# Kernel tuning notes

Measured on AMD Instinct MI355X. Metric: run time of the kernel, lower is better.

## Reference

```python
import jax, jax.numpy as jnp
import numpy as np

H = 512          # HIDDEN_DIM
W = 480          # WINDOWWIDTH
NL = 8           # NUMLABELS (output_dim)
STEPS = W // 15  # 32 decoder steps
ATT = W // 16    # 30 attention positions
B = 4            # window batch
L = 12           # per-frame sequence length
D_IN = 32        # input_dim
N = B * W        # 1920 frame sequences


def _lstm(x, Wih, Whh, bih, bhh):
    # x: [T, Bn, Din] -> per-step hidden/cell states [T, Bn, Hd] (torch LSTM gate order i,f,g,o)
    xp = x @ Wih.T + (bih + bhh)
    h0 = jnp.zeros((x.shape[1], Whh.shape[1]), x.dtype)
    def step(carry, xt):
        h, c = carry
        g = xt + h @ Whh.T
        i, f, gg, o = jnp.split(g, 4, axis=-1)
        c = jax.nn.sigmoid(f) * c + jax.nn.sigmoid(i) * jnp.tanh(gg)
        h = jax.nn.sigmoid(o) * jnp.tanh(c)
        return (h, c), (h, c)
    _, (hs, cs) = jax.lax.scan(step, (h0, h0), xp)
    return hs, cs


def _bilstm(x, Wf, Uf, bf, cf, Wb, Ub, bb, cb):
    # x: [Bt, T, D] batch_first; returns ([Bt, T, 2H], h_fwd_final, h_bwd_final)
    xt = jnp.swapaxes(x, 0, 1)
    hf, _ = _lstm(xt, Wf, Uf, bf, cf)
    hb, _ = _lstm(xt[::-1], Wb, Ub, bb, cb)
    out = jnp.concatenate([hf, hb[::-1]], axis=-1)
    return jnp.swapaxes(out, 0, 1), hf[-1], hb[-1]


def _forward(xs, xlengths, enc_Wih, enc_Whh, enc_bih, enc_bhh,
             penc_Wih_f, penc_Whh_f, penc_bih_f, penc_bhh_f,
             penc_Wih_b, penc_Whh_b, penc_bih_b, penc_bhh_b,
             attn_W, attn_b, comb_W, comb_b,
             gru_Wih, gru_Whh, gru_bih, gru_bhh, out_W, out_b):
    # frame-level encoder: packed sequences -> (h, c) at each sequence's true length
    hs, cs = _lstm(xs, enc_Wih, enc_Whh, enc_bih, enc_bhh)   # [L, N, H] each
    idx = xlengths - 1
    ar = jnp.arange(N)
    ctx = jnp.concatenate([hs[idx, ar], cs[idx, ar]], axis=-1)  # [N, 2H]
    ctx = ctx.reshape(B, W // 2, 4 * H)
    # pyramidal BiLSTM stack (dropout is identity at eval)
    out = ctx
    hf = hb = None
    for i in range(4):
        out, hf, hb = _bilstm(ctx, penc_Wih_f[i], penc_Whh_f[i], penc_bih_f[i], penc_bhh_f[i],
                              penc_Wih_b[i], penc_Whh_b[i], penc_bih_b[i], penc_bhh_b[i])
        if i < 3:
            ctx = out.reshape(B, W // (2 ** (i + 2)), 4 * H)
    enc_out = out                                   # [B, ATT, 2H]
    hidden0 = jnp.concatenate([hf, hb], axis=-1)    # [B, 2H]

    def dstep(carry, _):
        inp, h = carry                              # [B, NL], [B, 2H]
        aw = jax.nn.softmax(jnp.concatenate([inp, h], axis=-1) @ attn_W.T + attn_b, axis=-1)
        ctxv = jnp.einsum('bt,btd->bd', aw, enc_out)
        x = jax.nn.relu(jnp.concatenate([inp, ctxv], axis=-1) @ comb_W.T + comb_b)
        # torch GRU cell (gate order r, z, n)
        gi = x @ gru_Wih.T + gru_bih
        gh = h @ gru_Whh.T + gru_bhh
        ir, iz, inn = jnp.split(gi, 3, axis=-1)
        hr, hz, hn = jnp.split(gh, 3, axis=-1)
        r = jax.nn.sigmoid(ir + hr)
        z = jax.nn.sigmoid(iz + hz)
        n = jnp.tanh(inn + r * hn)
        hnew = (1.0 - z) * n + z * h
        logp = jax.nn.log_softmax(hnew @ out_W.T + out_b, axis=-1)
        return (logp, hnew), logp                   # free-running: next input = log-probs

    inp0 = jnp.zeros((B, NL), xs.dtype)
    _, outs = jax.lax.scan(dstep, (inp0, hidden0), None, length=STEPS)  # [STEPS, B, NL]
    return jnp.swapaxes(outs, 0, 1).reshape(B * STEPS, NL)


def setup_inputs() -> dict:
    key = jax.random.key(0)
    ks = jax.random.split(key, 24)
    s = 0.03
    def nrm(k, shape):
        return jax.random.normal(k, shape, dtype=jnp.float32) * s
    return {
        'xs': jax.random.normal(ks[0], (L, N, D_IN), dtype=jnp.float32),
        'xlengths': jax.random.randint(ks[1], (N,), 1, L + 1, dtype=jnp.int32),
        'enc_Wih': nrm(ks[2], (4 * H, D_IN)),
        'enc_Whh': nrm(ks[3], (4 * H, H)),
        'enc_bih': nrm(ks[4], (4 * H,)),
        'enc_bhh': nrm(ks[5], (4 * H,)),
        'penc_Wih_f': nrm(ks[6], (4, 4 * H, 4 * H)),
        'penc_Whh_f': nrm(ks[7], (4, 4 * H, H)),
        'penc_bih_f': nrm(ks[8], (4, 4 * H)),
        'penc_bhh_f': nrm(ks[9], (4, 4 * H)),
        'penc_Wih_b': nrm(ks[10], (4, 4 * H, 4 * H)),
        'penc_Whh_b': nrm(ks[11], (4, 4 * H, H)),
        'penc_bih_b': nrm(ks[12], (4, 4 * H)),
        'penc_bhh_b': nrm(ks[13], (4, 4 * H)),
        'attn_W': nrm(ks[14], (ATT, 2 * H + NL)),
        'attn_b': nrm(ks[15], (ATT,)),
        'comb_W': nrm(ks[16], (H, 2 * H + NL)),
        'comb_b': nrm(ks[17], (H,)),
        'gru_Wih': nrm(ks[18], (3 * 2 * H, H)),
        'gru_Whh': nrm(ks[19], (3 * 2 * H, 2 * H)),
        'gru_bih': nrm(ks[20], (3 * 2 * H,)),
        'gru_bhh': nrm(ks[21], (3 * 2 * H,)),
        'out_W': nrm(ks[22], (NL, 2 * H)),
        'out_b': nrm(ks[23], (NL,)),
    }


def reference(xs, xlengths, enc_Wih, enc_Whh, enc_bih, enc_bhh,
              penc_Wih_f, penc_Whh_f, penc_bih_f, penc_bhh_f,
              penc_Wih_b, penc_Whh_b, penc_bih_b, penc_bhh_b,
              attn_W, attn_b, comb_W, comb_b,
              gru_Wih, gru_Whh, gru_bih, gru_bhh, out_W, out_b):
    return _forward(xs, xlengths, enc_Wih, enc_Whh, enc_bih, enc_bhh,
                    penc_Wih_f, penc_Whh_f, penc_bih_f, penc_bhh_f,
                    penc_Wih_b, penc_Whh_b, penc_bih_b, penc_bhh_b,
                    attn_W, attn_b, comb_W, comb_b,
                    gru_Wih, gru_Whh, gru_bih, gru_bhh, out_W, out_b)
```

## Files before the change

kernel.cpp:

```cpp
#include <hip/hip_runtime.h>
#include <stdint.h>

typedef __attribute__((ext_vector_type(8))) __bf16 bf16x8;
typedef __attribute__((ext_vector_type(4))) float f32x4;
typedef __attribute__((ext_vector_type(4))) unsigned u32x4;

#define DEVI static __device__ __forceinline__
#define SENT 0xFFFFFFFFu

DEVI bf16x8 bzero8(){ bf16x8 r;
#pragma unroll
  for (int i=0;i<8;++i) r[i]=(__bf16)0.0f; return r; }

DEVI bf16x8 ld8(const __bf16* p){ return *(const bf16x8*)p; }
DEVI void st8(__bf16* p, bf16x8 v){ *(bf16x8*)p = v; }

DEVI f32x4 MFMA(bf16x8 a, bf16x8 b, f32x4 c){
  return __builtin_amdgcn_mfma_f32_16x16x32_bf16(a, b, c, 0, 0, 0);
}

DEVI float sigf(float x){ return 1.0f/(1.0f+__expf(-x)); }

DEVI void ast(unsigned* p, unsigned v){ __hip_atomic_store(p, v, __ATOMIC_RELAXED, __HIP_MEMORY_SCOPE_AGENT); }

DEVI unsigned packbf(float a, float b){
  union { __bf16 h[2]; unsigned u; } x; x.h[0]=(__bf16)a; x.h[1]=(__bf16)b; return x.u;
}
DEVI float bflo(unsigned u){ return __builtin_bit_cast(float, u<<16); }
DEVI float bfhi(unsigned u){ return __builtin_bit_cast(float, u & 0xffff0000u); }

DEVI unsigned bad4(u32x4 v){ return (v[0]==SENT)|(v[1]==SENT)|(v[2]==SENT)|(v[3]==SENT); }

DEVI u32x4 ald4(const void* p){
  u32x4 v;
  asm volatile("global_load_dwordx4 %0, %1, off sc0 sc1\n\ts_waitcnt vmcnt(0)"
               : "=&v"(v) : "v"(p) : "memory");
  return v;
}
DEVI u32x4 poll4(const void* p){
  u32x4 v = ald4(p);
  while (bad4(v)){ __builtin_amdgcn_s_sleep(1); v = ald4(p); }
  return v;
}
DEVI void ald4x2(const void* p, u32x4& a, u32x4& b){
  asm volatile("global_load_dwordx4 %0, %2, off sc0 sc1\n\t"
               "global_load_dwordx4 %1, %2, off offset:16 sc0 sc1\n\t"
               "s_waitcnt vmcnt(0)"
               : "=&v"(a), "=&v"(b) : "v"(p) : "memory");
}
DEVI void poll4x2(const void* p, u32x4& a, u32x4& b){
  ald4x2(p, a, b);
  while (bad4(a) | bad4(b)){ __builtin_amdgcn_s_sleep(1); ald4x2(p, a, b); }
}

DEVI void packGroup(const float* W, int Nsrc, int Kreal, int NT, __bf16* dst, long g){
  int kt = (int)(g / (NT*64));
  int rem = (int)(g % (NT*64));
  int nt = rem >> 6, ln = rem & 63;
  int row = nt*16 + (ln & 15);
  int col = kt*32 + ((ln >> 4) << 3);
  bf16x8 v = bzero8();
  if (row < Nsrc){
#pragma unroll
    for (int j=0;j<8;++j){ int c = col + j; if (c < Kreal) v[j] = (__bf16)W[(long)row*Kreal + c]; }
  }
  st8(dst + g*8, v);
}

DEVI void packGroupCat(const float* Wih, const float* Whh, __bf16* dst, long g){
  int kt = (int)(g / (128*64));
  int rem = (int)(g % (128*64));
  int nt = rem >> 6, ln = rem & 63;
  int prow = nt*16 + (ln & 15);
  int src = (prow & 3)*512 + (prow >> 2);
  int col = kt*32 + ((ln >> 4) << 3);
  bf16x8 v;
  if (col < 32){
#pragma unroll
    for (int j=0;j<8;++j) v[j] = (__bf16)Wih[(long)src*32 + col + j];
  } else {
#pragma unroll
    for (int j=0;j<8;++j) v[j] = (__bf16)Whh[(long)src*512 + (col-32) + j];
  }
  st8(dst + g*8, v);
}

__global__ void initK(unsigned* bar, unsigned* hb, unsigned* ctx, unsigned* xb){
  int g = blockIdx.x*256 + threadIdx.x;
  if (g < 3072){ bar[g] = 0u; return; }
  g -= 3072;
  if (g < 6144){ hb[2048 + g] = SENT; return; }
  g -= 6144;
  if (g < 8192){ ctx[g] = SENT; return; }
  g -= 8192;
  if (g < 4096){ xb[g] = SENT; return; }
}

__global__ void packSmallK(const float* __restrict__ xs, const float* __restrict__ eWih,
    const float* __restrict__ eWhh, const float* __restrict__ ebih, const float* __restrict__ ebhh,
    const float* __restrict__ attnW, const float* __restrict__ combW,
    __bf16* __restrict__ xsb, __bf16* __restrict__ wcatp, float* __restrict__ biasc,
    __bf16* __restrict__ attnp, __bf16* __restrict__ combp)
{
  long g = (long)blockIdx.x*blockDim.x + threadIdx.x;
  const long nWcat = 17L*128*64;
  const long nXs   = 92160;
  const long nBias = 2048;
  const long nAttn = 33L*2*64;
  const long nComb = 33L*32*64;
  if (g < nWcat){ packGroupCat(eWih, eWhh, wcatp, g); return; }
  g -= nWcat;
  if (g < nXs){
    const float* s = xs + g*8; bf16x8 v;
#pragma unroll
    for (int j=0;j<8;++j) v[j] = (__bf16)s[j];
    st8(xsb + g*8, v); return;
  }
  g -= nXs;
  if (g < nBias){ int src = ((int)g & 3)*512 + ((int)g >> 2); biasc[g] = ebih[src] + ebhh[src]; return; }
  g -= nBias;
  if (g < nAttn){ packGroup(attnW, 30, 1032, 2, attnp, g); return; }
  g -= nAttn;
  if (g < nComb){ packGroup(combW, 512, 1032, 32, combp, g); return; }
}

__global__ void packPencK(const float* __restrict__ Wf, const float* __restrict__ Wb,
    const float* __restrict__ bihf, const float* __restrict__ bhhf,
    const float* __restrict__ bihb, const float* __restrict__ bhhb,
    __bf16* __restrict__ pf, __bf16* __restrict__ pb, float* __restrict__ bsum,
    unsigned* __restrict__ hpy)
{
  long g = (long)blockIdx.x*blockDim.x + threadIdx.x;
  const long nW = 64L*128*64;
  if (g < nW){ packGroup(Wf, 2048, 2048, 128, pf, g); return; }
  g -= nW;
  if (g < nW){ packGroup(Wb, 2048, 2048, 128, pb, g); return; }
  g -= nW;
  if (g < 2048){ bsum[g] = bihf[g] + bhhf[g]; return; }
  g -= 2048;
  if (g < 2048){ bsum[2048+g] = bihb[g] + bhhb[g]; return; }
  g -= 2048;
  if (g < 8192){
    hpy[g] = ((g >> 10) & 3) ? SENT : 0u;
  }
}

__global__ __launch_bounds__(256, 1) void encStepK(
    const __bf16* __restrict__ xsb,
    __bf16* __restrict__ henc,
    float* __restrict__ cenc,
    const __bf16* __restrict__ wcatp,
    const float* __restrict__ biasc,
    const int* __restrict__ xlen,
    __bf16* __restrict__ ctx,
    int t)
{
  __shared__ float glds[64][260];
  const int tid = threadIdx.x;
  const int w = tid >> 6, ln = tid & 63;
  const int m0 = blockIdx.x * 64;
  const int nb = blockIdx.y;
  f32x4 acc[16];
#pragma unroll
  for (int i=0;i<16;++i) acc[i] = (f32x4){0.f,0.f,0.f,0.f};

  const int arow = m0 + w*16 + (ln & 15);
  const int kc = (ln >> 4) << 3;
  const int ktEnd = (t == 0) ? 1 : 17;
  for (int kt = 0; kt < ktEnd; ++kt){
    bf16x8 a;
    if (kt == 0) a = ld8(xsb + ((long)t*1920 + arow)*32 + kc);
    else         a = ld8(henc + (long)arow*512 + (kt-1)*32 + kc);
    const __bf16* bp = wcatp + (((long)kt*128 + nb*16)*64 + ln)*8;
#pragma unroll
    for (int n2 = 0; n2 < 16; ++n2){
      bf16x8 b = ld8(bp + (long)n2*512);
      acc[n2] = MFMA(a, b, acc[n2]);
    }
  }
  const int r4 = (ln >> 4) << 2;
#pragma unroll
  for (int n2 = 0; n2 < 16; ++n2){
#pragma unroll
    for (int r = 0; r < 4; ++r)
      glds[w*16 + r4 + r][n2*16 + (ln & 15)] = acc[n2][r];
  }
  __syncthreads();
  for (int it = 0; it < 16; ++it){
    int idx = tid + it*256;
    int mrow = idx >> 6, hcl = idx & 63;
    int n = m0 + mrow;
    int hcg = nb*64 + hcl;
    float ig = glds[mrow][hcl*4+0] + biasc[nb*256 + hcl*4+0];
    float fg = glds[mrow][hcl*4+1] + biasc[nb*256 + hcl*4+1];
    float gg = glds[mrow][hcl*4+2] + biasc[nb*256 + hcl*4+2];
    float og = glds[mrow][hcl*4+3] + biasc[nb*256 + hcl*4+3];
    float c_old = (t == 0) ? 0.0f : cenc[(long)n*512 + hcg];
    float cn = sigf(fg)*c_old + sigf(ig)*tanhf(gg);
    float h  = sigf(og)*tanhf(cn);
    cenc[(long)n*512 + hcg] = cn;
    henc[(long)n*512 + hcg] = (__bf16)h;
    if (xlen[n] - 1 == t){
      ctx[(long)n*1024 + hcg]       = (__bf16)h;
      ctx[(long)n*1024 + 512 + hcg] = (__bf16)cn;
    }
  }
}

__global__ __launch_bounds__(1024) void pencInK(
   const __bf16* __restrict__ inb,
   const __bf16* __restrict__ wpf, const __bf16* __restrict__ wpb,
   const float* __restrict__ bsum,
   float* __restrict__ xpf, float* __restrict__ xpb,
   int M)
{
  const int tid = threadIdx.x, ln = tid & 63, wv = tid >> 6;
  const int rg = wv >> 2, cg = wv & 3;
  const int dir = blockIdx.z;
  const int m0 = blockIdx.x*64 + rg*16;
  const int nb = blockIdx.y;
  const __bf16* wp = dir ? wpb : wpf;
  float* xp = dir ? xpb : xpf;
  const float* bs = bsum + dir*2048;
  f32x4 acc[4];
#pragma unroll
  for (int i=0;i<4;++i) acc[i] = (f32x4){0.f,0.f,0.f,0.f};
  const int arow = m0 + (ln & 15);
  const int kc = (ln >> 4) << 3;
  const bool aok = arow < M;
  for (int kt = 0; kt < 64; ++kt){
    bf16x8 a = aok ? ld8(inb + (long)arow*2048 + kt*32 + kc) : bzero8();
    const __bf16* bp = wp + (((long)kt*128 + nb*16 + cg*4)*64 + ln)*8;
#pragma unroll
    for (int q = 0; q < 4; ++q){
      bf16x8 b = ld8(bp + (long)q*512);
      acc[q] = MFMA(a, b, acc[q]);
    }
  }
  const int r4 = (ln >> 4) << 2;
#pragma unroll
  for (int q = 0; q < 4; ++q){
    int col = (nb*16 + cg*4 + q)*16 + (ln & 15);
#pragma unroll
    for (int r = 0; r < 4; ++r){
      int rowo = m0 + r4 + r;
      if (rowo < M) xp[(long)rowo*2048 + col] = acc[q][r] + bs[col];
    }
  }
}

__global__ __launch_bounds__(256, 1) void pyrRecK(
  const float* __restrict__ WhhF, const float* __restrict__ WhhB,
  const float* __restrict__ xpf, const float* __restrict__ xpb,
  __bf16* __restrict__ hbuf,
  __bf16* __restrict__ outb,
  float* __restrict__ outf,
  float* __restrict__ h0f, __bf16* __restrict__ h0b,
  int T, int isLast)
{
  __shared__ __align__(16) __bf16 WL[128*512];
  __shared__ __align__(16) __bf16 hsL[4*512];
  __shared__ float glds[4][4][32];
  const int tid = threadIdx.x, ln = tid & 63, w = tid >> 6;
  const int bk = blockIdx.x;
  const int dir = bk >> 4, slot = bk & 15;
  const int hc0 = slot * 32;
  const float* Whh = dir ? WhhB : WhhF;
  const float* xp  = dir ? xpb : xpf;
  unsigned* hbu = (unsigned*)hbuf;

  for (int it = 0; it < 32; ++it){
    int g = it*256 + tid;
    int rho = g >> 6, c8 = g & 63;
    int gate = rho >> 5, hcl = rho & 31;
    const float* src = Whh + ((long)(gate*512 + hc0 + hcl))*512 + c8*8;
    bf16x8 v;
#pragma unroll
    for (int j=0;j<8;++j) v[j] = (__bf16)src[j];
    int off = (rho*1024 + c8*16) ^ ((rho & 7) << 4);
    st8((__bf16*)((char*)WL + off), v);
  }

  float cv = 0.0f;
  const int arow = ln & 15;
  const int kc = (ln >> 4) << 3;
  const int rho0 = w*32 + (ln & 15);
  const int rho1 = rho0 + 16;
  for (int t = 0; t < T; ++t){
    int cur = t & 3, nxt = (t+1) & 3, clr = (t+2) & 3;
    int pos = dir ? (T-1-t) : t;
    float x0=0.f, x1=0.f, x2=0.f, x3=0.f;
    if (tid < 128){
      const float* xr = xp + ((long)((tid>>5)*T + pos))*2048 + hc0 + (tid & 31);
      x0 = xr[0]; x1 = xr[512]; x2 = xr[1024]; x3 = xr[1536];
    }
    if (tid < 128 && !(tid & 1)){
      int b = tid >> 5, hcl = tid & 31;
      ast(hbu + ((size_t)(dir*4 + clr)*4 + b)*256 + ((hc0 + hcl) >> 1), SENT);
    }
    {
      u32x4 v = poll4((const char*)hbuf + (size_t)(dir*4 + cur)*4096 + tid*16);
      ((u32x4*)hsL)[tid] = v;
    }
    __syncthreads();
    f32x4 a0 = {0.f,0.f,0.f,0.f}, a1 = {0.f,0.f,0.f,0.f};
#pragma unroll
    for (int kt = 0; kt < 16; ++kt){
      bf16x8 a = (arow < 4) ? ld8(hsL + arow*512 + kt*32 + kc) : bzero8();
      int k2 = (kt*32 + kc)*2;
      bf16x8 b0 = ld8((__bf16*)((char*)WL + ((rho0*1024 + k2) ^ ((rho0 & 7) << 4))));
      bf16x8 b1 = ld8((__bf16*)((char*)WL + ((rho1*1024 + k2) ^ ((rho1 & 7) << 4))));
      a0 = MFMA(a, b0, a0);
      a1 = MFMA(a, b1, a1);
    }
    __syncthreads();
    if (ln < 16){
#pragma unroll
      for (int r=0;r<4;++r){ glds[w][r][ln] = a0[r]; glds[w][r][16+ln] = a1[r]; }
    }
    __syncthreads();
    if (tid < 128){
      int b = tid >> 5, hcl = tid & 31, hcg = hc0 + hcl;
      float ig = glds[0][b][hcl] + x0;
      float fg = glds[1][b][hcl] + x1;
      float gg = glds[2][b][hcl] + x2;
      float og = glds[3][b][hcl] + x3;
      cv = sigf(fg)*cv + sigf(ig)*tanhf(gg);
      float h = sigf(og)*tanhf(cv);
      float hn = __shfl_down(h, 1);
      if (!(hcl & 1))
        ast(hbu + ((size_t)(dir*4 + nxt)*4 + b)*256 + (hcg >> 1), packbf(h, hn));
      if (!isLast){
        outb[((long)(b*T + pos))*1024 + dir*512 + hcg] = (__bf16)h;
      } else {
        outf[((long)(b*T + pos))*1024 + dir*512 + hcg] = h;
        if (t == T-1){
          h0f[b*1024 + dir*512 + hcg] = h;
          h0b[b*1024 + dir*512 + hcg] = (__bf16)h;
        }
      }
    }
  }
}

DEVI bf16x8 dfrag(const __bf16* base, const __bf16* inp, int row, int kt, int kc, int stride){
  if (row >= 4) return bzero8();
  int k = kt*32 + kc;
  if (k == 0) return ld8(inp + row*8);
  int off = k - 8;
  return (off < 1024) ? ld8(base + row*stride + off) : bzero8();
}

__global__ __launch_bounds__(256, 1) void decoderK(
  const float* __restrict__ gWih,
  const float* __restrict__ gWhh,
  const float* __restrict__ gbih, const float* __restrict__ gbhh,
  const float* __restrict__ combBias, const float* __restrict__ attnBias,
  const float* __restrict__ outW, const float* __restrict__ outBias,
  const __bf16* __restrict__ attnP, const __bf16* __restrict__ combP,
  const float* __restrict__ encOut,
  const float* __restrict__ h0f,
  __bf16* __restrict__ HB,
  __bf16* __restrict__ CTXB,
  __bf16* __restrict__ XB,
  float* __restrict__ dout)
{
  __shared__ __align__(16) __bf16 giL[96*512];
  __shared__ __align__(16) __bf16 outWL[8*1024];
  __shared__ __align__(16) __bf16 hL[4*1024];
  __shared__ __align__(16) __bf16 ctxvL[4][1056];
  __shared__ __align__(16) __bf16 xL[4][528];
  __shared__ __bf16 encOutL[4][30][32];
  __shared__ __align__(16) __bf16 inpL[32];
  __shared__ float awL[4][30];
  __shared__ float redL[4][8];
  __shared__ float ghL[3][4][32];
  __shared__ float giO[3][4][32];
  __shared__ float combL[4][4][16];
  __shared__ float biL[3][32], bhL[3][32];
  __shared__ float abL[30], cbL[16];

  const int tid = threadIdx.x, ln = tid & 63, w = tid >> 6;
  const int slot = blockIdx.x;
  const int hc0 = slot * 32;
  unsigned* HBu = (unsigned*)HB;
  unsigned* CTXu = (unsigned*)CTXB;
  unsigned* XBu = (unsigned*)XB;

  for (int it = 0; it < 24; ++it){
    int g = it*256 + tid;
    int rho = g >> 6, c8 = g & 63;
    int gate = rho >> 5, r = rho & 31;
    const float* s = gWih + ((long)(gate*1024 + hc0 + r))*512 + c8*8;
    bf16x8 v;
#pragma unroll
    for (int j=0;j<8;++j) v[j] = (__bf16)s[j];
    st8((__bf16*)((char*)giL + ((rho*1024 + c8*16) ^ ((rho & 7) << 4))), v);
  }
  for (int it = 0; it < 32; ++it){
    int g = it*256 + tid;
    outWL[g] = (__bf16)outW[g];
  }
  for (int idx = tid; idx < 3840; idx += 256){
    int b = idx/960, rem = idx%960;
    int t2 = rem >> 5, dl = rem & 31;
    encOutL[b][t2][dl] = (__bf16)encOut[((long)b*30 + t2)*1024 + hc0 + dl];
  }
  if (tid < 96){
    int g2 = tid >> 5, l = tid & 31;
    biL[g2][l] = gbih[g2*1024 + hc0 + l];
    bhL[g2][l] = gbhh[g2*1024 + hc0 + l];
  }
  if (tid < 30) abL[tid] = attnBias[tid];
  if (tid < 16) cbL[tid] = combBias[slot*16 + tid];

  const int row = ln & 15, kc = (ln >> 4) << 3;
  bf16x8 bigF[66];
  if (w == 0){
#pragma unroll
    for (int nt = 0; nt < 2; ++nt)
#pragma unroll
      for (int kt = 0; kt < 33; ++kt)
        bigF[nt*33 + kt] = ld8(attnP + (((size_t)kt*2 + nt)*64 + ln)*8);
  } else {
    int gate = w - 1;
#pragma unroll
    for (int nt = 0; nt < 2; ++nt)
#pragma unroll
      for (int kt = 0; kt < 32; ++kt){
        const float* s = gWhh + ((long)(gate*1024 + hc0 + nt*16 + row))*1024 + kt*32 + kc;
        bf16x8 v;
#pragma unroll
        for (int j=0;j<8;++j) v[j] = (__bf16)s[j];
        bigF[nt*33 + kt] = v;
      }
  }
  const int kt0c = (w == 0) ? 0 : (w*8 + 1);
  const int nkt = (w == 0) ? 9 : 8;
  bf16x8 combF[9];
#pragma unroll
  for (int i = 0; i < 9; ++i)
    combF[i] = (i < nkt) ? ld8(combP + (((size_t)(kt0c+i)*32 + slot)*64 + ln)*8) : bzero8();

  float hold = 0.f;
  if (tid < 128) hold = h0f[(tid>>5)*1024 + hc0 + (tid & 31)];
  __syncthreads();

  for (int s = 0; s <= 32; ++s){
    int cur = s & 3, nxt = (s+1) & 3, clr = (s+2) & 3;
    if (tid < 64){
      int b = tid >> 4, i = tid & 15;
      ast(HBu  + ((size_t)clr*4 + b)*512 + (hc0 >> 1) + i, SENT);
      ast(CTXu + ((size_t)clr*4 + b)*512 + (hc0 >> 1) + i, SENT);
    }
    if (tid < 32){
      int b = tid >> 3, i = tid & 7;
      ast(XBu + ((size_t)clr*4 + b)*256 + ((slot*16) >> 1) + i, SENT);
    }
    {
      u32x4 q0, q1;
      poll4x2((const char*)HB + (size_t)cur*8192 + tid*32, q0, q1);
      ((u32x4*)hL)[tid*2]   = q0;
      ((u32x4*)hL)[tid*2+1] = q1;
    }
    __syncthreads();
    if (s == 0){
      if (tid < 32) inpL[tid] = (__bf16)0.0f;
      __syncthreads();
    } else {
      int o = tid >> 3, sl = tid & 7;
      int b = o >> 3, l = o & 7;
      const unsigned* hlp = (const unsigned*)hL + b*512 + sl*64;
      const unsigned* wlp = (const unsigned*)outWL + l*512 + sl*64;
      float p = 0.f;
      for (int kk = 0; kk < 64; ++kk){
        unsigned u = hlp[kk], t2 = wlp[kk];
        p += bflo(u)*bflo(t2) + bfhi(u)*bfhi(t2);
      }
      p += __shfl_down(p, 4);
      p += __shfl_down(p, 2);
      p += __shfl_down(p, 1);
      if (sl == 0) redL[b][l] = p + outBias[l];
      __syncthreads();
      if (tid < 4){
        float m = redL[tid][0];
        for (int l2=1;l2<8;++l2) m = fmaxf(m, redL[tid][l2]);
        float sum = 0.f;
        for (int l2=0;l2<8;++l2) sum += __expf(redL[tid][l2]-m);
        float lse = m + __logf(sum);
        for (int l2=0;l2<8;++l2){
          float lp = redL[tid][l2] - lse;
          inpL[tid*8 + l2] = (__bf16)lp;
          if (slot == 0) dout[((long)tid*32 + (s-1))*8 + l2] = lp;
        }
      }
      __syncthreads();
    }
    if (s == 32) break;

    if (w == 0){
      f32x4 a0 = {0.f,0.f,0.f,0.f}, a1 = {0.f,0.f,0.f,0.f};
#pragma unroll
      for (int kt = 0; kt < 33; ++kt){
        bf16x8 a = dfrag(hL, inpL, row, kt, kc, 1024);
        a0 = MFMA(a, bigF[kt], a0);
        a1 = MFMA(a, bigF[33+kt], a1);
      }
      if (ln < 16){
#pragma unroll
        for (int r=0;r<4;++r) awL[r][ln] = a0[r] + abL[ln];
        if (16 + ln < 30){
#pragma unroll
          for (int r=0;r<4;++r) awL[r][16+ln] = a1[r] + abL[16+ln];
        }
      }
    } else {
      f32x4 a0 = {0.f,0.f,0.f,0.f}, a1 = {0.f,0.f,0.f,0.f};
#pragma unroll
      for (int kt = 0; kt < 32; ++kt){
        int k = kt*32 + kc;
        bf16x8 a = (row < 4) ? ld8(hL + row*1024 + k) : bzero8();
        a0 = MFMA(a, bigF[kt], a0);
        a1 = MFMA(a, bigF[33+kt], a1);
      }
      if (ln < 16){
        int gate = w - 1;
#pragma unroll
        for (int r=0;r<4;++r){
          ghL[gate][r][ln] = a0[r];
          ghL[gate][r][16+ln] = a1[r];
        }
      }
    }
    __syncthreads();
    if (tid < 4){
      float m = awL[tid][0];
      for (int t2=1;t2<30;++t2) m = fmaxf(m, awL[tid][t2]);
      float sum = 0.f;
      for (int t2=0;t2<30;++t2){ float e = __expf(awL[tid][t2]-m); awL[tid][t2] = e; sum += e; }
      float inv = 1.0f/sum;
      for (int t2=0;t2<30;++t2) awL[tid][t2] *= inv;
    }
    __syncthreads();
    if (tid < 128){
      int b = tid >> 5, dl = tid & 31;
      float sum = 0.f;
      for (int t2=0;t2<30;++t2) sum += awL[b][t2]*(float)encOutL[b][t2][dl];
      float sn = __shfl_down(sum, 1);
      if (!(dl & 1))
        ast(CTXu + ((size_t)cur*4 + b)*512 + ((hc0 + dl) >> 1), packbf(sum, sn));
    }
    {
      u32x4 q0, q1;
      poll4x2((const char*)CTXB + (size_t)cur*8192 + tid*32, q0, q1);
      u32x4* dst = (u32x4*)((char*)&ctxvL[0][0] + (tid>>6)*2112 + (tid&63)*32);
      dst[0] = q0; dst[1] = q1;
    }
    __syncthreads();
    {
      f32x4 acc = {0.f,0.f,0.f,0.f};
#pragma unroll
      for (int i = 0; i < 9; ++i){
        if (i < nkt){
          bf16x8 a = dfrag(&ctxvL[0][0], inpL, row, kt0c+i, kc, 1056);
          acc = MFMA(a, combF[i], acc);
        }
      }
      if (ln < 16){
#pragma unroll
        for (int r=0;r<4;++r) combL[w][r][ln] = acc[r];
      }
    }
    __syncthreads();
    if (tid < 64){
      int r = tid >> 4, l = tid & 15, col = slot*16 + l;
      float x = combL[0][r][l] + combL[1][r][l] + combL[2][r][l] + combL[3][r][l] + cbL[l];
      x = fmaxf(x, 0.0f);
      float xn = __shfl_down(x, 1);
      if (!(l & 1))
        ast(XBu + ((size_t)cur*4 + r)*256 + (col >> 1), packbf(x, xn));
    }
    {
      u32x4 v = poll4((const char*)XB + (size_t)cur*4096 + tid*16);
      u32x4* dst = (u32x4*)((char*)&xL[0][0] + (tid>>6)*1056 + (tid&63)*16);
      dst[0] = v;
    }
    __syncthreads();
    if (w >= 1){
      int gate = w - 1;
      f32x4 a0 = {0.f,0.f,0.f,0.f}, a1 = {0.f,0.f,0.f,0.f};
#pragma unroll
      for (int kt = 0; kt < 16; ++kt){
        int k = kt*32 + kc;
        bf16x8 a = (row < 4) ? ld8(&xL[row][k]) : bzero8();
        int r0 = gate*32 + row, r1 = r0 + 16;
        bf16x8 b0 = ld8((__bf16*)((char*)giL + ((r0*1024 + k*2) ^ ((r0 & 7) << 4))));
        bf16x8 b1 = ld8((__bf16*)((char*)giL + ((r1*1024 + k*2) ^ ((r1 & 7) << 4))));
        a0 = MFMA(a, b0, a0);
        a1 = MFMA(a, b1, a1);
      }
      if (ln < 16){
#pragma unroll
        for (int r=0;r<4;++r){
          giO[gate][r][ln] = a0[r] + biL[gate][ln];
          giO[gate][r][16+ln] = a1[r] + biL[gate][16+ln];
        }
      }
    }
    __syncthreads();
    if (tid < 128){
      int b = tid >> 5, l = tid & 31, hcg = hc0 + l;
      float rr = sigf(giO[0][b][l] + ghL[0][b][l] + bhL[0][l]);
      float zz = sigf(giO[1][b][l] + ghL[1][b][l] + bhL[1][l]);
      float nn = tanhf(giO[2][b][l] + rr*(ghL[2][b][l] + bhL[2][l]));
      float hnew = (1.0f - zz)*nn + zz*hold;
      hold = hnew;
      float h2 = __shfl_down(hnew, 1);
      if (!(l & 1))
        ast(HBu + ((size_t)nxt*4 + b)*512 + (hcg >> 1), packbf(hnew, h2));
    }
  }
}

static const size_t O_BAR   = 0;
static const size_t O_XSB   = 12288;
static const size_t O_WCATP = 1486848;
static const size_t O_BIASC = 3715072;
static const size_t O_HENC  = 3723264;
static const size_t O_CENC  = 5689344;
static const size_t O_CTX   = 9621504;
static const size_t O_WIHPF = 13553664;
static const size_t O_WIHPB = 21942272;
static const size_t O_BSUM  = 30330880;
static const size_t O_XPF   = 30347264;
static const size_t O_XPB   = 38211584;
static const size_t O_HPYR  = 46075904;
static const size_t O_OUTA  = 46108672;
static const size_t O_OUTB  = 48074752;
static const size_t O_ENCO  = 49057792;
static const size_t O_H0F   = 49549312;
static const size_t O_HB    = 49565696;
static const size_t O_CTXB  = 49598464;
static const size_t O_XB    = 49631232;
static const size_t O_ATTNP = 49647616;
static const size_t O_COMBP = 49715200;

extern "C" void kernel_launch(void* const* d_in, const int* in_sizes, int n_in,
                              void* d_out, int out_size, void* d_ws, size_t ws_size,
                              hipStream_t stream)
{
  const float* xs    = (const float*)d_in[0];
  const int*   xlen  = (const int*)d_in[1];
  const float* eWih  = (const float*)d_in[2];
  const float* eWhh  = (const float*)d_in[3];
  const float* ebih  = (const float*)d_in[4];
  const float* ebhh  = (const float*)d_in[5];
  const float* pWihF = (const float*)d_in[6];
  const float* pWhhF = (const float*)d_in[7];
  const float* pbihF = (const float*)d_in[8];
  const float* pbhhF = (const float*)d_in[9];
  const float* pWihB = (const float*)d_in[10];
  const float* pWhhB = (const float*)d_in[11];
  const float* pbihB = (const float*)d_in[12];
  const float* pbhhB = (const float*)d_in[13];
  const float* attnW = (const float*)d_in[14];
  const float* attnb = (const float*)d_in[15];
  const float* combW = (const float*)d_in[16];
  const float* combb = (const float*)d_in[17];
  const float* gWih  = (const float*)d_in[18];
  const float* gWhh  = (const float*)d_in[19];
  const float* gbih  = (const float*)d_in[20];
  const float* gbhh  = (const float*)d_in[21];
  const float* outW  = (const float*)d_in[22];
  const float* outb  = (const float*)d_in[23];

  char* ws = (char*)d_ws;
  unsigned* BARU  = (unsigned*)(ws + O_BAR);
  __bf16* XSB     = (__bf16*)(ws + O_XSB);
  __bf16* WCATP   = (__bf16*)(ws + O_WCATP);
  float*  BIASC   = (float*)(ws + O_BIASC);
  __bf16* HENC    = (__bf16*)(ws + O_HENC);
  float*  CENC    = (float*)(ws + O_CENC);
  __bf16* CTX     = (__bf16*)(ws + O_CTX);
  __bf16* WIHPF   = (__bf16*)(ws + O_WIHPF);
  __bf16* WIHPB   = (__bf16*)(ws + O_WIHPB);
  float*  BSUM    = (float*)(ws + O_BSUM);
  float*  XPF     = (float*)(ws + O_XPF);
  float*  XPB     = (float*)(ws + O_XPB);
  __bf16* HPYR    = (__bf16*)(ws + O_HPYR);
  __bf16* OUTA    = (__bf16*)(ws + O_OUTA);
  __bf16* OUTB    = (__bf16*)(ws + O_OUTB);
  float*  ENCO    = (float*)(ws + O_ENCO);
  float*  H0F     = (float*)(ws + O_H0F);
  __bf16* HB      = (__bf16*)(ws + O_HB);
  __bf16* CTXB    = (__bf16*)(ws + O_CTXB);
  __bf16* XB      = (__bf16*)(ws + O_XB);
  __bf16* ATTNP   = (__bf16*)(ws + O_ATTNP);
  __bf16* COMBP   = (__bf16*)(ws + O_COMBP);

  initK<<<84, 256, 0, stream>>>(BARU, (unsigned*)HB, (unsigned*)CTXB, (unsigned*)XB);
  packSmallK<<<1193, 256, 0, stream>>>(xs, eWih, eWhh, ebih, ebhh, attnW, combW,
      XSB, WCATP, BIASC, ATTNP, COMBP);

  for (int t = 0; t < 12; ++t)
    encStepK<<<dim3(30, 8), 256, 0, stream>>>(XSB, HENC, CENC, WCATP, BIASC, xlen, CTX, t);

  const int Ts[4] = {240, 120, 60, 30};
  const __bf16* ins[4] = {CTX, OUTA, OUTB, OUTA};
  __bf16* outs[4] = {OUTA, OUTB, OUTA, OUTB};
  for (int L = 0; L < 4; ++L){
    int T = Ts[L];
    packPencK<<<4145, 256, 0, stream>>>(pWihF + (long)L*2048*2048, pWihB + (long)L*2048*2048,
        pbihF + L*2048, pbhhF + L*2048, pbihB + L*2048, pbhhB + L*2048,
        WIHPF, WIHPB, BSUM, (unsigned*)HPYR);
    int MB = (4*T + 63)/64;
    pencInK<<<dim3(MB, 8, 2), 1024, 0, stream>>>(ins[L], WIHPF, WIHPB, BSUM, XPF, XPB, 4*T);
    pyrRecK<<<32, 256, 0, stream>>>(pWhhF + (long)L*2048*512, pWhhB + (long)L*2048*512,
        XPF, XPB, HPYR, outs[L], ENCO, H0F, HB, T, (L==3) ? 1 : 0);
  }

  decoderK<<<32, 256, 0, stream>>>(gWih, gWhh, gbih, gbhh, combb, attnb, outW, outb,
      ATTNP, COMBP, ENCO, H0F, HB, CTXB, XB, (float*)d_out);
}
```

Measured before the change: 2.256 ms.

## Hold pyramid recurrent weights in registers, prefetch inputs, double-buffer hidden state

The pyramid BiLSTM recurrent kernel now keeps its Whh slice in registers as pre-packed MFMA fragments, replacing the per-block fp32-to-bf16 conversion into LDS and the LDS weight reads on every step. A new stage in the pack kernel writes these fragments into the workspace region the finished encoder no longer uses. The recurrent loop double-buffers the hidden-state LDS copy, which removes one barrier per step, and prefetches the next step's input projections while the MFMAs run. The sentinel clears move after the barrier in both the pyramid and decoder loops. The trade-off is much higher register pressure (32 bf16x8 fragments per lane) and a risk of spills.

After: 2.117 ms. -6.2%, faster.

```diff
diff --git a/kernel.cpp b/kernel.cpp
--- a/kernel.cpp
+++ b/kernel.cpp
@@ -125,10 +125,11 @@
 }
 
 __global__ void packPencK(const float* __restrict__ Wf, const float* __restrict__ Wb,
+    const float* __restrict__ WhF, const float* __restrict__ WhB,
     const float* __restrict__ bihf, const float* __restrict__ bhhf,
     const float* __restrict__ bihb, const float* __restrict__ bhhb,
     __bf16* __restrict__ pf, __bf16* __restrict__ pb, float* __restrict__ bsum,
-    unsigned* __restrict__ hpy)
+    __bf16* __restrict__ pwhh, unsigned* __restrict__ hpy)
 {
   long g = (long)blockIdx.x*blockDim.x + threadIdx.x;
   const long nW = 64L*128*64;
@@ -142,6 +143,24 @@
   g -= 2048;
   if (g < 8192){
     hpy[g] = ((g >> 10) & 3) ? SENT : 0u;
+    return;
+  }
+  g -= 8192;
+  if (g < 262144){
+    int lane = (int)(g & 63);
+    int f    = (int)((g >> 6) & 31);
+    int w    = (int)((g >> 11) & 3);
+    int slot = (int)((g >> 13) & 15);
+    int dir  = (int)((g >> 17) & 1);
+    int kt = f >> 1, nt = f & 1;
+    int row16 = lane & 15, kch = lane >> 4;
+    int srow = w*512 + slot*32 + nt*16 + row16;
+    int scol = kt*32 + kch*8;
+    const float* W = dir ? WhB : WhF;
+    bf16x8 v;
+#pragma unroll
+    for (int j=0;j<8;++j) v[j] = (__bf16)W[(long)srow*512 + scol + j];
+    st8(pwhh + g*8, v);
   }
 }
 
@@ -250,7 +269,7 @@
 }
 
 __global__ __launch_bounds__(256, 1) void pyrRecK(
-  const float* __restrict__ WhhF, const float* __restrict__ WhhB,
+  const __bf16* __restrict__ pwhh,
   const float* __restrict__ xpf, const float* __restrict__ xpb,
   __bf16* __restrict__ hbuf,
   __bf16* __restrict__ outb,
@@ -258,62 +277,58 @@
   float* __restrict__ h0f, __bf16* __restrict__ h0b,
   int T, int isLast)
 {
-  __shared__ __align__(16) __bf16 WL[128*512];
-  __shared__ __align__(16) __bf16 hsL[4*512];
+  __shared__ __align__(16) __bf16 hsL[2][4*512];
   __shared__ float glds[4][4][32];
   const int tid = threadIdx.x, ln = tid & 63, w = tid >> 6;
   const int bk = blockIdx.x;
   const int dir = bk >> 4, slot = bk & 15;
   const int hc0 = slot * 32;
-  const float* Whh = dir ? WhhB : WhhF;
-  const float* xp  = dir ? xpb : xpf;
+  const float* xp = dir ? xpb : xpf;
   unsigned* hbu = (unsigned*)hbuf;
 
-  for (int it = 0; it < 32; ++it){
-    int g = it*256 + tid;
-    int rho = g >> 6, c8 = g & 63;
-    int gate = rho >> 5, hcl = rho & 31;
-    const float* src = Whh + ((long)(gate*512 + hc0 + hcl))*512 + c8*8;
-    bf16x8 v;
-#pragma unroll
-    for (int j=0;j<8;++j) v[j] = (__bf16)src[j];
-    int off = (rho*1024 + c8*16) ^ ((rho & 7) << 4);
-    st8((__bf16*)((char*)WL + off), v);
-  }
-
-  float cv = 0.0f;
+  bf16x8 BF[32];
+  {
+    const __bf16* wb = pwhh + ((((size_t)(dir*16 + slot)*4 + w)*32)*64 + ln)*8;
+#pragma unroll
+    for (int f = 0; f < 32; ++f) BF[f] = ld8(wb + (size_t)f*512);
+  }
+
   const int arow = ln & 15;
   const int kc = (ln >> 4) << 3;
-  const int rho0 = w*32 + (ln & 15);
-  const int rho1 = rho0 + 16;
+  float cv = 0.0f;
+  float x0=0.f,x1=0.f,x2=0.f,x3=0.f;
+  if (tid < 128){
+    int pos0 = dir ? (T-1) : 0;
+    const float* xr = xp + ((size_t)((tid>>5)*T + pos0))*2048 + hc0 + (tid & 31);
+    x0 = xr[0]; x1 = xr[512]; x2 = xr[1024]; x3 = xr[1536];
+  }
+
   for (int t = 0; t < T; ++t){
     int cur = t & 3, nxt = (t+1) & 3, clr = (t+2) & 3;
     int pos = dir ? (T-1-t) : t;
-    float x0=0.f, x1=0.f, x2=0.f, x3=0.f;
-    if (tid < 128){
-      const float* xr = xp + ((long)((tid>>5)*T + pos))*2048 + hc0 + (tid & 31);
-      x0 = xr[0]; x1 = xr[512]; x2 = xr[1024]; x3 = xr[1536];
-    }
-    if (tid < 128 && !(tid & 1)){
-      int b = tid >> 5, hcl = tid & 31;
-      ast(hbu + ((size_t)(dir*4 + clr)*4 + b)*256 + ((hc0 + hcl) >> 1), SENT);
-    }
     {
       u32x4 v = poll4((const char*)hbuf + (size_t)(dir*4 + cur)*4096 + tid*16);
-      ((u32x4*)hsL)[tid] = v;
-    }
-    __syncthreads();
+      ((u32x4*)hsL[t & 1])[tid] = v;
+    }
+    __syncthreads();
+    if (tid < 64){
+      int b = tid >> 4, i = tid & 15;
+      ast(hbu + ((size_t)(dir*4 + clr)*4 + b)*256 + (hc0 >> 1) + i, SENT);
+    }
+    const __bf16* hs = hsL[t & 1];
     f32x4 a0 = {0.f,0.f,0.f,0.f}, a1 = {0.f,0.f,0.f,0.f};
 #pragma unroll
     for (int kt = 0; kt < 16; ++kt){
-      bf16x8 a = (arow < 4) ? ld8(hsL + arow*512 + kt*32 + kc) : bzero8();
-      int k2 = (kt*32 + kc)*2;
-      bf16x8 b0 = ld8((__bf16*)((char*)WL + ((rho0*1024 + k2) ^ ((rho0 & 7) << 4))));
-      bf16x8 b1 = ld8((__bf16*)((char*)WL + ((rho1*1024 + k2) ^ ((rho1 & 7) << 4))));
-      a0 = MFMA(a, b0, a0);
-      a1 = MFMA(a, b1, a1);
-    }
-    __syncthreads();
+      bf16x8 a = (arow < 4) ? ld8(hs + arow*512 + kt*32 + kc) : bzero8();
+      a0 = MFMA(a, BF[kt*2+0], a0);
+      a1 = MFMA(a, BF[kt*2+1], a1);
+    }
+    float xn0=0.f,xn1=0.f,xn2=0.f,xn3=0.f;
+    if (t+1 < T && tid < 128){
+      int pos2 = dir ? (T-2-t) : (t+1);
+      const float* xr = xp + ((size_t)((tid>>5)*T + pos2))*2048 + hc0 + (tid & 31);
+      xn0 = xr[0]; xn1 = xr[512]; xn2 = xr[1024]; xn3 = xr[1536];
+    }
     if (ln < 16){
 #pragma unroll
       for (int r=0;r<4;++r){ glds[w][r][ln] = a0[r]; glds[w][r][16+ln] = a1[r]; }
@@ -340,6 +355,7 @@
         }
       }
     }
+    x0=xn0; x1=xn1; x2=xn2; x3=xn3;
   }
 }
 
@@ -448,15 +464,6 @@
 
   for (int s = 0; s <= 32; ++s){
     int cur = s & 3, nxt = (s+1) & 3, clr = (s+2) & 3;
-    if (tid < 64){
-      int b = tid >> 4, i = tid & 15;
-      ast(HBu  + ((size_t)clr*4 + b)*512 + (hc0 >> 1) + i, SENT);
-      ast(CTXu + ((size_t)clr*4 + b)*512 + (hc0 >> 1) + i, SENT);
-    }
-    if (tid < 32){
-      int b = tid >> 3, i = tid & 7;
-      ast(XBu + ((size_t)clr*4 + b)*256 + ((slot*16) >> 1) + i, SENT);
-    }
     {
       u32x4 q0, q1;
       poll4x2((const char*)HB + (size_t)cur*8192 + tid*32, q0, q1);
@@ -464,6 +471,15 @@
       ((u32x4*)hL)[tid*2+1] = q1;
     }
     __syncthreads();
+    if (tid < 64){
+      int b = tid >> 4, i = tid & 15;
+      ast(HBu  + ((size_t)clr*4 + b)*512 + (hc0 >> 1) + i, SENT);
+      ast(CTXu + ((size_t)clr*4 + b)*512 + (hc0 >> 1) + i, SENT);
+    }
+    if (tid < 32){
+      int b = tid >> 3, i = tid & 7;
+      ast(XBu + ((size_t)clr*4 + b)*256 + ((slot*16) >> 1) + i, SENT);
+    }
     if (s == 0){
       if (tid < 32) inpL[tid] = (__bf16)0.0f;
       __syncthreads();
@@ -627,6 +643,7 @@
 static const size_t O_WCATP = 1486848;
 static const size_t O_BIASC = 3715072;
 static const size_t O_HENC  = 3723264;
+static const size_t O_PWHH  = 3723264;
 static const size_t O_CENC  = 5689344;
 static const size_t O_CTX   = 9621504;
 static const size_t O_WIHPF = 13553664;
@@ -680,6 +697,7 @@
   __bf16* WCATP   = (__bf16*)(ws + O_WCATP);
   float*  BIASC   = (float*)(ws + O_BIASC);
   __bf16* HENC    = (__bf16*)(ws + O_HENC);
+  __bf16* PWHH    = (__bf16*)(ws + O_PWHH);
   float*  CENC    = (float*)(ws + O_CENC);
   __bf16* CTX     = (__bf16*)(ws + O_CTX);
   __bf16* WIHPF   = (__bf16*)(ws + O_WIHPF);
@@ -710,13 +728,14 @@
   __bf16* outs[4] = {OUTA, OUTB, OUTA, OUTB};
   for (int L = 0; L < 4; ++L){
     int T = Ts[L];
-    packPencK<<<4145, 256, 0, stream>>>(pWihF + (long)L*2048*2048, pWihB + (long)L*2048*2048,
+    packPencK<<<5168, 256, 0, stream>>>(pWihF + (long)L*2048*2048, pWihB + (long)L*2048*2048,
+        pWhhF + (long)L*2048*512, pWhhB + (long)L*2048*512,
         pbihF + L*2048, pbhhF + L*2048, pbihB + L*2048, pbhhB + L*2048,
-        WIHPF, WIHPB, BSUM, (unsigned*)HPYR);
+        WIHPF, WIHPB, BSUM, PWHH, (unsigned*)HPYR);
     int MB = (4*T + 63)/64;
     pencInK<<<dim3(MB, 8, 2), 1024, 0, stream>>>(ins[L], WIHPF, WIHPB, BSUM, XPF, XPB, 4*T);
-    pyrRecK<<<32, 256, 0, stream>>>(pWhhF + (long)L*2048*512, pWhhB + (long)L*2048*512,
-        XPF, XPB, HPYR, outs[L], ENCO, H0F, HB, T, (L==3) ? 1 : 0);
+    pyrRecK<<<32, 256, 0, stream>>>(PWHH, XPF, XPB, HPYR, outs[L], ENCO, H0F, HB,
+        T, (L==3) ? 1 : 0);
   }
 
   decoderK<<<32, 256, 0, stream>>>(gWih, gWhh, gbih, gbhh, combb, attnb, outW, outb,
```
